# Optimization experiments

Measured on AMD Instinct MI355X. Metric: run time of the kernel, lower is better.

## Reference

```python
import jax, jax.numpy as jnp
import numpy as np

B, F, D, H, E, K = 4, 2048, 1024, 2048, 8, 2  # batch, frames, dim, expert hidden, n_experts, top_k


def setup_inputs() -> dict:
    key = jax.random.key(0)
    ks = jax.random.split(key, 9)
    sc = lambda k, shape, fan_in: (jax.random.normal(k, shape, jnp.float32) * (fan_in ** -0.5))
    return {
        "x": jax.random.normal(ks[0], (B, F, D), jnp.float32),
        # router: Linear(D,D) -> SiLU -> Linear(D,E)
        "rw1": sc(ks[1], (D, D), D),
        "rb1": jnp.zeros((D,), jnp.float32),
        "rw2": sc(ks[2], (D, E), D),
        "rb2": jnp.zeros((E,), jnp.float32),
        # experts: E x (Linear(D,H) -> SiLU -> Linear(H,D))
        "ew1": sc(ks[3], (E, D, H), D),
        "eb1": jnp.zeros((E, H), jnp.float32),
        "ew2": sc(ks[4], (E, H, D), H),
        "eb2": jnp.zeros((E, D), jnp.float32),
    }


def reference(x, rw1, rb1, rw2, rb2, ew1, eb1, ew2, eb2):
    b, f, d = x.shape
    t = x.reshape(b * f, d)                                   # [T, D]
    # router (eval mode: no topk noise)
    logits = jax.nn.silu(t @ rw1 + rb1) @ rw2 + rb2            # [T, E]
    vals, idx = jax.lax.top_k(logits, K)                       # [T, K]
    rows = jnp.arange(t.shape[0])[:, None]
    masked = jnp.full_like(logits, -jnp.inf).at[rows, idx].set(vals)
    w = jax.nn.softmax(masked, axis=1)                         # [T, E], nonzero only on top-k
    # dense per-expert FFN, then weighted combine (residual: y starts as x)
    eh = jax.nn.silu(jnp.einsum('td,edh->teh', t, ew1) + eb1[None])   # [T, E, H]
    eo = jnp.einsum('teh,ehd->ted', eh, ew2) + eb2[None]              # [T, E, D]
    y = t + jnp.einsum('te,ted->td', w, eo)
    return y.reshape(b, f, d)
```

## Files before the change

### kernel.cpp

```cpp
#include <hip/hip_runtime.h>
#include <hip/hip_bf16.h>
#include <cstdint>
#include <cstddef>

#define T_TOK 8192
#define DDIM  1024
#define HDIM  2048
#define NEXP  8
#define TOPK  2
#define KAUG  (3 * DDIM)

typedef short bf16x8 __attribute__((ext_vector_type(8)));
typedef float f32x4  __attribute__((ext_vector_type(4)));

__device__ __forceinline__ unsigned short f2bf(float f) {
  union { float f; unsigned u; } v; v.f = f;
  unsigned r = v.u + 0x7FFFu + ((v.u >> 16) & 1u);
  return (unsigned short)(r >> 16);
}
__device__ __forceinline__ float bf2f(unsigned short h) {
  union { unsigned u; float f; } v; v.u = ((unsigned)h) << 16;
  return v.f;
}
__device__ __forceinline__ float silu_fast(float v) {
  return v / (1.0f + __expf(-v));
}
__device__ __forceinline__ float silu_precise(float v) {
  return v / (1.0f + expf(-v));
}

__device__ __forceinline__ void gload16(const unsigned short* g, unsigned short* l) {
  __builtin_amdgcn_global_load_lds(
      (const __attribute__((address_space(1))) unsigned int*)g,
      (__attribute__((address_space(3))) unsigned int*)l,
      16, 0, 0);
}

__global__ void split_x_kernel(const float* __restrict__ in,
                               unsigned short* __restrict__ xaug, int n4) {
  int i = blockIdx.x * blockDim.x + threadIdx.x;
  if (i >= n4) return;
  float4 v = ((const float4*)in)[i];
  int t = i / (DDIM / 4);
  int kc = (i % (DDIM / 4)) * 4;
  float f[4] = {v.x, v.y, v.z, v.w};
  ushort4 hi, lo;
  unsigned short h[4], l[4];
#pragma unroll
  for (int j = 0; j < 4; j++) {
    h[j] = f2bf(f[j]);
    l[j] = f2bf(f[j] - bf2f(h[j]));
  }
  hi.x = h[0]; hi.y = h[1]; hi.z = h[2]; hi.w = h[3];
  lo.x = l[0]; lo.y = l[1]; lo.z = l[2]; lo.w = l[3];
  *(ushort4*)&xaug[(size_t)t * KAUG + kc] = hi;
  *(ushort4*)&xaug[(size_t)t * KAUG + DDIM + kc] = hi;
  *(ushort4*)&xaug[(size_t)t * KAUG + 2 * DDIM + kc] = lo;
}

__global__ __launch_bounds__(256) void split_w_kernel(
    const float* __restrict__ in, unsigned short* __restrict__ waug) {
  __shared__ float tile[32][33];
  int c0 = blockIdx.x * 32, r0 = blockIdx.y * 32;
  int tx = threadIdx.x & 31, ty = threadIdx.x >> 5;
#pragma unroll
  for (int i = 0; i < 32; i += 8)
    tile[ty + i][tx] = in[(size_t)(r0 + ty + i) * DDIM + (c0 + tx)];
  __syncthreads();
#pragma unroll
  for (int i = 0; i < 32; i += 8) {
    float v = tile[tx][ty + i];
    unsigned short h = f2bf(v);
    unsigned short l = f2bf(v - bf2f(h));
    int n = c0 + ty + i, k = r0 + tx;
    waug[(size_t)n * KAUG + k] = h;
    waug[(size_t)n * KAUG + DDIM + k] = l;
    waug[(size_t)n * KAUG + 2 * DDIM + k] = h;
  }
}

__global__ __launch_bounds__(256) void transpose_conv_kernel(
    const float* __restrict__ in, unsigned short* __restrict__ out, int R, int C) {
  __shared__ float tile[32][33];
  const int z = blockIdx.z;
  const float* src = in + (size_t)z * R * C;
  unsigned short* dst = out + (size_t)z * R * C;
  int c0 = blockIdx.x * 32, r0 = blockIdx.y * 32;
  int tx = threadIdx.x & 31, ty = threadIdx.x >> 5;
#pragma unroll
  for (int i = 0; i < 32; i += 8)
    tile[ty + i][tx] = src[(size_t)(r0 + ty + i) * C + (c0 + tx)];
  __syncthreads();
#pragma unroll
  for (int i = 0; i < 32; i += 8)
    dst[(size_t)(c0 + ty + i) * R + (r0 + tx)] = f2bf(tile[tx][ty + i]);
}

__global__ void zero_small_kernel(int* __restrict__ counts, int* __restrict__ cursors) {
  int i = threadIdx.x;
  if (i < NEXP) { counts[i] = 0; cursors[i] = 0; }
}

template <int EPI>
__global__ __launch_bounds__(256) void gemm_mfma(
    const unsigned short* __restrict__ Abase,
    const unsigned short* __restrict__ Btbase,
    const float* __restrict__ bias,
    float* __restrict__ outF,
    unsigned short* __restrict__ outBf,
    const int* __restrict__ toks,
    const int* __restrict__ offs, const int* __restrict__ cnts,
    int N, int KD, int Astride, int numE, int nTiles, int mCap) {
  const int id = blockIdx.x;
  const int e = id % numE;
  const int r = id / numE;
  const int n0 = (r % nTiles) * 128;
  const int mb = r / nTiles;

  int ne = T_TOK, off = 0;
  if (EPI != 0) { ne = cnts[e]; off = offs[e]; }

  const unsigned short* Bt = Btbase + (size_t)e * N * KD;
  const unsigned short* A = (EPI == 2) ? (Abase + (size_t)off * Astride) : Abase;

  __shared__ unsigned short As[2][128][32];
  __shared__ unsigned short Bs[2][128][32];

  const int tid  = threadIdx.x;
  const int lane = tid & 63, wid = tid >> 6;
  const int wm = wid >> 1, wn = wid & 1;
  const int quad = lane >> 4, l16 = lane & 15;

  const int rowS0 = tid >> 2;
  const int kc0 = (tid & 3) * 8;

  const size_t brow0 = (size_t)(n0 + rowS0) * KD;
  const size_t brow1 = brow0 + (size_t)64 * KD;
  const int nIter = KD / 32;
  const int mStride = mCap * 128;

  for (int m0 = mb * 128; m0 < ne; m0 += mStride) {
    size_t arow0, arow1;
    if (EPI == 1) {
      int p0 = m0 + rowS0, p1 = m0 + rowS0 + 64;
      int t0 = (p0 < ne) ? toks[off + p0] : 0;
      int t1 = (p1 < ne) ? toks[off + p1] : 0;
      arow0 = (size_t)t0 * Astride;
      arow1 = (size_t)t1 * Astride;
    } else if (EPI == 2) {
      arow0 = (size_t)min(m0 + rowS0, ne - 1) * Astride;
      arow1 = (size_t)min(m0 + rowS0 + 64, ne - 1) * Astride;
    } else {
      arow0 = (size_t)(m0 + rowS0) * Astride;
      arow1 = arow0 + (size_t)64 * Astride;
    }

    f32x4 zf = {0.f, 0.f, 0.f, 0.f};
    f32x4 acc[4][4];
#pragma unroll
    for (int mi = 0; mi < 4; mi++)
#pragma unroll
      for (int ni = 0; ni < 4; ni++) acc[mi][ni] = zf;

    {
      unsigned short* a0 = &As[0][0][0] + wid * 512;
      unsigned short* b0 = &Bs[0][0][0] + wid * 512;
      gload16(A + arow0 + kc0, a0);
      gload16(A + arow1 + kc0, a0 + 2048);
      gload16(Bt + brow0 + kc0, b0);
      gload16(Bt + brow1 + kc0, b0 + 2048);
    }

    for (int k = 0; k < nIter; k++) {
      const int cur = k & 1;
      if (k + 1 < nIter) {
        const int nk = (k + 1) * 32;
        unsigned short* a0 = &As[cur ^ 1][0][0] + wid * 512;
        unsigned short* b0 = &Bs[cur ^ 1][0][0] + wid * 512;
        gload16(A + arow0 + nk + kc0, a0);
        gload16(A + arow1 + nk + kc0, a0 + 2048);
        gload16(Bt + brow0 + nk + kc0, b0);
        gload16(Bt + brow1 + nk + kc0, b0 + 2048);
        __builtin_amdgcn_s_waitcnt(0x0F74);
      } else {
        __builtin_amdgcn_s_waitcnt(0x0F70);
      }
      __builtin_amdgcn_s_barrier();
      bf16x8 af[4], bfr[4];
#pragma unroll
      for (int mi = 0; mi < 4; mi++)
        af[mi] = *(const bf16x8*)&As[cur][wm * 64 + mi * 16 + l16][quad * 8];
#pragma unroll
      for (int ni = 0; ni < 4; ni++)
        bfr[ni] = *(const bf16x8*)&Bs[cur][wn * 64 + ni * 16 + l16][quad * 8];
#pragma unroll
      for (int mi = 0; mi < 4; mi++)
#pragma unroll
        for (int ni = 0; ni < 4; ni++)
          acc[mi][ni] = __builtin_amdgcn_mfma_f32_16x16x32_bf16(
              af[mi], bfr[ni], acc[mi][ni], 0, 0, 0);
      __builtin_amdgcn_s_barrier();
    }

#pragma unroll
    for (int mi = 0; mi < 4; mi++) {
      const int prow_base = wm * 64 + mi * 16 + quad * 4;
#pragma unroll
      for (int rr = 0; rr < 4; rr++) {
        const int p = m0 + prow_base + rr;
        if (EPI != 0 && p >= ne) continue;
#pragma unroll
        for (int ni = 0; ni < 4; ni++) {
          const int col = n0 + wn * 64 + ni * 16 + l16;
          float v = acc[mi][ni][rr] + bias[(size_t)e * N + col];
          if (EPI == 0) {
            outF[(size_t)p * N + col] = silu_precise(v);
          } else if (EPI == 1) {
            outBf[(size_t)(off + p) * N + col] = f2bf(silu_fast(v));
          } else {
            outBf[(size_t)(off + p) * N + col] = f2bf(v);
          }
        }
      }
    }
  }
}

__global__ __launch_bounds__(256) void router2_kernel(
    const float* __restrict__ rh, const float* __restrict__ rw2,
    const float* __restrict__ rb2, float* __restrict__ logits) {
  int t = blockIdx.x * 4 + (threadIdx.x >> 6);
  int lane = threadIdx.x & 63;
  const float* row = rh + (size_t)t * DDIM;
  float acc[NEXP];
#pragma unroll
  for (int e = 0; e < NEXP; e++) acc[e] = 0.f;
  for (int k = lane; k < DDIM; k += 64) {
    float v = row[k];
    const float* w = rw2 + (size_t)k * NEXP;
#pragma unroll
    for (int e = 0; e < NEXP; e++) acc[e] += v * w[e];
  }
#pragma unroll
  for (int e = 0; e < NEXP; e++) {
#pragma unroll
    for (int off = 32; off > 0; off >>= 1) acc[e] += __shfl_xor(acc[e], off, 64);
  }
#pragma unroll
  for (int e = 0; e < NEXP; e++)
    if (lane == e) logits[(size_t)t * NEXP + e] = acc[e] + rb2[e];
}

__global__ void topk_kernel(const float* __restrict__ logits,
                            int* __restrict__ idx2, float* __restrict__ w2arr,
                            int* __restrict__ counts) {
  int t = blockIdx.x * blockDim.x + threadIdx.x;
  if (t >= T_TOK) return;
  float l[NEXP];
#pragma unroll
  for (int e = 0; e < NEXP; e++) l[e] = logits[(size_t)t * NEXP + e];
  int i1 = 0; float v1 = l[0];
#pragma unroll
  for (int e = 1; e < NEXP; e++)
    if (l[e] > v1) { v1 = l[e]; i1 = e; }
  int i2 = -1; float v2 = -3.4e38f;
#pragma unroll
  for (int e = 0; e < NEXP; e++)
    if (e != i1 && l[e] > v2) { v2 = l[e]; i2 = e; }
  float ex = expf(v2 - v1);
  float wa = 1.f / (1.f + ex);
  float wb = ex / (1.f + ex);
  idx2[t * 2] = i1; idx2[t * 2 + 1] = i2;
  w2arr[t * 2] = wa; w2arr[t * 2 + 1] = wb;
  atomicAdd(&counts[i1], 1);
  atomicAdd(&counts[i2], 1);
}

__global__ void prefix_kernel(const int* __restrict__ counts, int* __restrict__ offs) {
  if (threadIdx.x == 0 && blockIdx.x == 0) {
    int s = 0;
    for (int e = 0; e < NEXP; e++) { offs[e] = s; s += counts[e]; }
  }
}

__global__ void scatter_kernel(const int* __restrict__ idx2,
                               const int* __restrict__ offs, int* __restrict__ cursors,
                               int* __restrict__ toks, int* __restrict__ posArr) {
  int t = blockIdx.x * blockDim.x + threadIdx.x;
  if (t >= T_TOK) return;
#pragma unroll
  for (int j = 0; j < TOPK; j++) {
    int e = idx2[t * 2 + j];
    int pos = atomicAdd(&cursors[e], 1);
    int s = offs[e] + pos;
    toks[s] = t;
    posArr[t * 2 + j] = s;
  }
}

__global__ __launch_bounds__(256) void combine_kernel(
    const float* __restrict__ x, const unsigned short* __restrict__ eo,
    const int* __restrict__ posArr, const float* __restrict__ w2arr,
    float* __restrict__ y) {
  const int t = blockIdx.x;
  const int d = threadIdx.x * 4;
  const int s0 = posArr[t * 2], s1 = posArr[t * 2 + 1];
  const float w0 = w2arr[t * 2], w1 = w2arr[t * 2 + 1];
  float4 xv = *(const float4*)&x[(size_t)t * DDIM + d];
  ushort4 a = *(const ushort4*)&eo[(size_t)s0 * DDIM + d];
  ushort4 b = *(const ushort4*)&eo[(size_t)s1 * DDIM + d];
  float4 o;
  o.x = xv.x + w0 * bf2f(a.x) + w1 * bf2f(b.x);
  o.y = xv.y + w0 * bf2f(a.y) + w1 * bf2f(b.y);
  o.z = xv.z + w0 * bf2f(a.z) + w1 * bf2f(b.z);
  o.w = xv.w + w0 * bf2f(a.w) + w1 * bf2f(b.w);
  *(float4*)&y[(size_t)t * DDIM + d] = o;
}

extern "C" void kernel_launch(void* const* d_in, const int* in_sizes, int n_in,
                              void* d_out, int out_size, void* d_ws, size_t ws_size,
                              hipStream_t stream) {
  (void)in_sizes; (void)n_in; (void)out_size; (void)ws_size;
  const float* x   = (const float*)d_in[0];
  const float* rw1 = (const float*)d_in[1];
  const float* rb1 = (const float*)d_in[2];
  const float* rw2 = (const float*)d_in[3];
  const float* rb2 = (const float*)d_in[4];
  const float* ew1 = (const float*)d_in[5];
  const float* eb1 = (const float*)d_in[6];
  const float* ew2 = (const float*)d_in[7];
  const float* eb2 = (const float*)d_in[8];
  float* y = (float*)d_out;

  char* ws = (char*)d_ws;
  size_t o = 0;
  auto alloc = [&](size_t bytes) {
    size_t r = o;
    o += (bytes + 255) & ~(size_t)255;
    return r;
  };
  unsigned short* xaug  = (unsigned short*)(ws + alloc((size_t)T_TOK * KAUG * 2));
  unsigned short* waug  = (unsigned short*)(ws + alloc((size_t)DDIM * KAUG * 2));
  unsigned short* ew1t  = (unsigned short*)(ws + alloc((size_t)NEXP * HDIM * DDIM * 2));
  unsigned short* ew2t  = (unsigned short*)(ws + alloc((size_t)NEXP * DDIM * HDIM * 2));
  float*          rh    = (float*)(ws + alloc((size_t)T_TOK * DDIM * 4));
  float*          logits= (float*)(ws + alloc((size_t)T_TOK * NEXP * 4));
  int*            idx2  = (int*)(ws + alloc((size_t)T_TOK * 2 * 4));
  float*          w2    = (float*)(ws + alloc((size_t)T_TOK * 2 * 4));
  int*            toks  = (int*)(ws + alloc((size_t)T_TOK * TOPK * 4));
  int*            posArr= (int*)(ws + alloc((size_t)T_TOK * TOPK * 4));
  int*            counts= (int*)(ws + alloc(256));
  int*            cursors=(int*)(ws + alloc(256));
  int*            offs  = (int*)(ws + alloc(256));
  unsigned short* ehb   = (unsigned short*)(ws + alloc((size_t)T_TOK * TOPK * HDIM * 2));
  unsigned short* eo    = (unsigned short*)(ws + alloc((size_t)T_TOK * TOPK * DDIM * 2));

  zero_small_kernel<<<1, 64, 0, stream>>>(counts, cursors);

  const int n4 = T_TOK * DDIM / 4;
  split_x_kernel<<<(n4 + 255) / 256, 256, 0, stream>>>(x, xaug, n4);
  split_w_kernel<<<dim3(DDIM / 32, DDIM / 32), 256, 0, stream>>>(rw1, waug);
  transpose_conv_kernel<<<dim3(HDIM / 32, DDIM / 32, NEXP), 256, 0, stream>>>(ew1, ew1t, DDIM, HDIM);
  transpose_conv_kernel<<<dim3(DDIM / 32, HDIM / 32, NEXP), 256, 0, stream>>>(ew2, ew2t, HDIM, DDIM);

  gemm_mfma<0><<<512, 256, 0, stream>>>(
      xaug, waug, rb1, rh, nullptr, nullptr, nullptr, nullptr,
      DDIM, KAUG, KAUG, 1, 8, 64);
  router2_kernel<<<T_TOK / 4, 256, 0, stream>>>(rh, rw2, rb2, logits);
  topk_kernel<<<T_TOK / 256, 256, 0, stream>>>(logits, idx2, w2, counts);
  prefix_kernel<<<1, 64, 0, stream>>>(counts, offs);
  scatter_kernel<<<T_TOK / 256, 256, 0, stream>>>(idx2, offs, cursors, toks, posArr);

  gemm_mfma<1><<<8 * 16 * 16, 256, 0, stream>>>(
      xaug, ew1t, eb1, nullptr, ehb, toks, offs, counts,
      HDIM, DDIM, KAUG, NEXP, 16, 16);
  gemm_mfma<2><<<8 * 8 * 32, 256, 0, stream>>>(
      ehb, ew2t, eb2, nullptr, eo, nullptr, offs, counts,
      DDIM, HDIM, HDIM, NEXP, 8, 32);
  combine_kernel<<<T_TOK, 256, 0, stream>>>(x, eo, posArr, w2, y);
}
```

Baseline: 804.9 us.

## Use plain bf16 router GEMM with fp32 fixup for near-tie tokens

Drops the three-term split-bf16 emulation of the fp32 router GEMM and runs it in plain bf16, which cuts the router GEMM K dimension by a factor of three and shrinks the x/weight staging buffers. To keep expert selection correct, tokens whose second and third logits fall within a small margin are flagged and recomputed in full fp32 by a new fixup kernel, which patches the indices, weights and counts. The prefix kernel is removed and offsets are recomputed inline from counts. This risks mis-routing tokens whose bf16 error exceeds the tie margin, and the fixup cost grows with the number of flagged tokens.

After: 1.078 ms. 1.34x slower.

```diff
diff --git a/kernel.cpp b/kernel.cpp
--- a/kernel.cpp
+++ b/kernel.cpp
@@ -8,7 +8,7 @@
 #define HDIM  2048
 #define NEXP  8
 #define TOPK  2
-#define KAUG  (3 * DDIM)
+#define TIE_DELTA 0.05f
 
 typedef short bf16x8 __attribute__((ext_vector_type(8)));
 typedef float f32x4  __attribute__((ext_vector_type(4)));
@@ -36,47 +36,14 @@
       16, 0, 0);
 }
 
-__global__ void split_x_kernel(const float* __restrict__ in,
-                               unsigned short* __restrict__ xaug, int n4) {
+__global__ void conv_x_kernel(const float* __restrict__ in,
+                              unsigned short* __restrict__ out, int n4) {
   int i = blockIdx.x * blockDim.x + threadIdx.x;
   if (i >= n4) return;
   float4 v = ((const float4*)in)[i];
-  int t = i / (DDIM / 4);
-  int kc = (i % (DDIM / 4)) * 4;
-  float f[4] = {v.x, v.y, v.z, v.w};
-  ushort4 hi, lo;
-  unsigned short h[4], l[4];
-#pragma unroll
-  for (int j = 0; j < 4; j++) {
-    h[j] = f2bf(f[j]);
-    l[j] = f2bf(f[j] - bf2f(h[j]));
-  }
-  hi.x = h[0]; hi.y = h[1]; hi.z = h[2]; hi.w = h[3];
-  lo.x = l[0]; lo.y = l[1]; lo.z = l[2]; lo.w = l[3];
-  *(ushort4*)&xaug[(size_t)t * KAUG + kc] = hi;
-  *(ushort4*)&xaug[(size_t)t * KAUG + DDIM + kc] = hi;
-  *(ushort4*)&xaug[(size_t)t * KAUG + 2 * DDIM + kc] = lo;
-}
-
-__global__ __launch_bounds__(256) void split_w_kernel(
-    const float* __restrict__ in, unsigned short* __restrict__ waug) {
-  __shared__ float tile[32][33];
-  int c0 = blockIdx.x * 32, r0 = blockIdx.y * 32;
-  int tx = threadIdx.x & 31, ty = threadIdx.x >> 5;
-#pragma unroll
-  for (int i = 0; i < 32; i += 8)
-    tile[ty + i][tx] = in[(size_t)(r0 + ty + i) * DDIM + (c0 + tx)];
-  __syncthreads();
-#pragma unroll
-  for (int i = 0; i < 32; i += 8) {
-    float v = tile[tx][ty + i];
-    unsigned short h = f2bf(v);
-    unsigned short l = f2bf(v - bf2f(h));
-    int n = c0 + ty + i, k = r0 + tx;
-    waug[(size_t)n * KAUG + k] = h;
-    waug[(size_t)n * KAUG + DDIM + k] = l;
-    waug[(size_t)n * KAUG + 2 * DDIM + k] = h;
-  }
+  ushort4 o;
+  o.x = f2bf(v.x); o.y = f2bf(v.y); o.z = f2bf(v.z); o.w = f2bf(v.w);
+  ((ushort4*)out)[i] = o;
 }
 
 __global__ __launch_bounds__(256) void transpose_conv_kernel(
@@ -96,9 +63,11 @@
     dst[(size_t)(c0 + ty + i) * R + (r0 + tx)] = f2bf(tile[tx][ty + i]);
 }
 
-__global__ void zero_small_kernel(int* __restrict__ counts, int* __restrict__ cursors) {
+__global__ void zero_small_kernel(int* __restrict__ counts, int* __restrict__ cursors,
+                                  int* __restrict__ flagCnt) {
   int i = threadIdx.x;
   if (i < NEXP) { counts[i] = 0; cursors[i] = 0; }
+  if (i == NEXP) *flagCnt = 0;
 }
 
 template <int EPI>
@@ -109,7 +78,7 @@
     float* __restrict__ outF,
     unsigned short* __restrict__ outBf,
     const int* __restrict__ toks,
-    const int* __restrict__ offs, const int* __restrict__ cnts,
+    const int* __restrict__ cnts,
     int N, int KD, int Astride, int numE, int nTiles, int mCap) {
   const int id = blockIdx.x;
   const int e = id % numE;
@@ -118,7 +87,13 @@
   const int mb = r / nTiles;
 
   int ne = T_TOK, off = 0;
-  if (EPI != 0) { ne = cnts[e]; off = offs[e]; }
+  if (EPI != 0) {
+    for (int q = 0; q < NEXP; q++) {
+      int c = cnts[q];
+      if (q < e) off += c;
+      if (q == e) ne = c;
+    }
+  }
 
   const unsigned short* Bt = Btbase + (size_t)e * N * KD;
   const unsigned short* A = (EPI == 2) ? (Abase + (size_t)off * Astride) : Abase;
@@ -253,7 +228,8 @@
 
 __global__ void topk_kernel(const float* __restrict__ logits,
                             int* __restrict__ idx2, float* __restrict__ w2arr,
-                            int* __restrict__ counts) {
+                            int* __restrict__ counts,
+                            int* __restrict__ flagList, int* __restrict__ flagCnt) {
   int t = blockIdx.x * blockDim.x + threadIdx.x;
   if (t >= T_TOK) return;
   float l[NEXP];
@@ -267,6 +243,10 @@
 #pragma unroll
   for (int e = 0; e < NEXP; e++)
     if (e != i1 && l[e] > v2) { v2 = l[e]; i2 = e; }
+  float v3 = -3.4e38f;
+#pragma unroll
+  for (int e = 0; e < NEXP; e++)
+    if (e != i1 && e != i2 && l[e] > v3) v3 = l[e];
   float ex = expf(v2 - v1);
   float wa = 1.f / (1.f + ex);
   float wb = ex / (1.f + ex);
@@ -274,27 +254,95 @@
   w2arr[t * 2] = wa; w2arr[t * 2 + 1] = wb;
   atomicAdd(&counts[i1], 1);
   atomicAdd(&counts[i2], 1);
-}
-
-__global__ void prefix_kernel(const int* __restrict__ counts, int* __restrict__ offs) {
-  if (threadIdx.x == 0 && blockIdx.x == 0) {
-    int s = 0;
-    for (int e = 0; e < NEXP; e++) { offs[e] = s; s += counts[e]; }
+  if (v2 - v3 < TIE_DELTA) {
+    int pos = atomicAdd(flagCnt, 1);
+    flagList[pos] = t;
+  }
+}
+
+__global__ __launch_bounds__(256) void fixup_kernel(
+    const float* __restrict__ x, const float* __restrict__ rw1,
+    const float* __restrict__ rb1, const float* __restrict__ rw2,
+    const float* __restrict__ rb2,
+    const int* __restrict__ flagList, const int* __restrict__ flagCnt,
+    int* __restrict__ idx2, float* __restrict__ w2arr, int* __restrict__ counts) {
+  __shared__ float xs[DDIM];
+  __shared__ float part[4][NEXP];
+  const int n = *flagCnt;
+  const int tid = threadIdx.x;
+  const int lane = tid & 63, wid = tid >> 6;
+  for (int i = blockIdx.x; i < n; i += gridDim.x) {
+    const int t = flagList[i];
+    for (int k = tid; k < DDIM; k += 256) xs[k] = x[(size_t)t * DDIM + k];
+    __syncthreads();
+    const int j0 = tid * 4;
+    float h0 = rb1[j0], h1 = rb1[j0 + 1], h2 = rb1[j0 + 2], h3 = rb1[j0 + 3];
+    for (int k = 0; k < DDIM; k++) {
+      float xv = xs[k];
+      float4 wv = *(const float4*)(rw1 + (size_t)k * DDIM + j0);
+      h0 += xv * wv.x; h1 += xv * wv.y; h2 += xv * wv.z; h3 += xv * wv.w;
+    }
+    h0 = silu_precise(h0); h1 = silu_precise(h1);
+    h2 = silu_precise(h2); h3 = silu_precise(h3);
+    float acc[NEXP];
+#pragma unroll
+    for (int e = 0; e < NEXP; e++) {
+      acc[e] = h0 * rw2[(size_t)j0 * NEXP + e] + h1 * rw2[(size_t)(j0 + 1) * NEXP + e]
+             + h2 * rw2[(size_t)(j0 + 2) * NEXP + e] + h3 * rw2[(size_t)(j0 + 3) * NEXP + e];
+    }
+#pragma unroll
+    for (int e = 0; e < NEXP; e++)
+#pragma unroll
+      for (int off = 32; off > 0; off >>= 1) acc[e] += __shfl_xor(acc[e], off, 64);
+    if (lane == 0)
+#pragma unroll
+      for (int e = 0; e < NEXP; e++) part[wid][e] = acc[e];
+    __syncthreads();
+    if (tid == 0) {
+      float l[NEXP];
+#pragma unroll
+      for (int e = 0; e < NEXP; e++)
+        l[e] = rb2[e] + part[0][e] + part[1][e] + part[2][e] + part[3][e];
+      int i1 = 0; float v1 = l[0];
+#pragma unroll
+      for (int e = 1; e < NEXP; e++)
+        if (l[e] > v1) { v1 = l[e]; i1 = e; }
+      int i2 = -1; float v2 = -3.4e38f;
+#pragma unroll
+      for (int e = 0; e < NEXP; e++)
+        if (e != i1 && l[e] > v2) { v2 = l[e]; i2 = e; }
+      float ex = expf(v2 - v1);
+      float wa = 1.f / (1.f + ex);
+      float wb = ex / (1.f + ex);
+      int o0 = idx2[t * 2], o1 = idx2[t * 2 + 1];
+      bool same = ((o0 == i1 && o1 == i2) || (o0 == i2 && o1 == i1));
+      if (!same) {
+        atomicSub(&counts[o0], 1); atomicSub(&counts[o1], 1);
+        atomicAdd(&counts[i1], 1); atomicAdd(&counts[i2], 1);
+      }
+      idx2[t * 2] = i1; idx2[t * 2 + 1] = i2;
+      w2arr[t * 2] = wa; w2arr[t * 2 + 1] = wb;
+    }
+    __syncthreads();
   }
 }
 
 __global__ void scatter_kernel(const int* __restrict__ idx2,
-                               const int* __restrict__ offs, int* __restrict__ cursors,
+                               const int* __restrict__ counts, int* __restrict__ cursors,
                                int* __restrict__ toks, int* __restrict__ posArr) {
   int t = blockIdx.x * blockDim.x + threadIdx.x;
   if (t >= T_TOK) return;
+  int offs[NEXP];
+  int s = 0;
+#pragma unroll
+  for (int e = 0; e < NEXP; e++) { offs[e] = s; s += counts[e]; }
 #pragma unroll
   for (int j = 0; j < TOPK; j++) {
     int e = idx2[t * 2 + j];
     int pos = atomicAdd(&cursors[e], 1);
-    int s = offs[e] + pos;
-    toks[s] = t;
-    posArr[t * 2 + j] = s;
+    int sl = offs[e] + pos;
+    toks[sl] = t;
+    posArr[t * 2 + j] = sl;
   }
 }
 
@@ -339,8 +387,8 @@
     o += (bytes + 255) & ~(size_t)255;
     return r;
   };
-  unsigned short* xaug  = (unsigned short*)(ws + alloc((size_t)T_TOK * KAUG * 2));
-  unsigned short* waug  = (unsigned short*)(ws + alloc((size_t)DDIM * KAUG * 2));
+  unsigned short* xb    = (unsigned short*)(ws + alloc((size_t)T_TOK * DDIM * 2));
+  unsigned short* w1t   = (unsigned short*)(ws + alloc((size_t)DDIM * DDIM * 2));
   unsigned short* ew1t  = (unsigned short*)(ws + alloc((size_t)NEXP * HDIM * DDIM * 2));
   unsigned short* ew2t  = (unsigned short*)(ws + alloc((size_t)NEXP * DDIM * HDIM * 2));
   float*          rh    = (float*)(ws + alloc((size_t)T_TOK * DDIM * 4));
@@ -349,33 +397,35 @@
   float*          w2    = (float*)(ws + alloc((size_t)T_TOK * 2 * 4));
   int*            toks  = (int*)(ws + alloc((size_t)T_TOK * TOPK * 4));
   int*            posArr= (int*)(ws + alloc((size_t)T_TOK * TOPK * 4));
+  int*            flagL = (int*)(ws + alloc((size_t)T_TOK * 4));
   int*            counts= (int*)(ws + alloc(256));
   int*            cursors=(int*)(ws + alloc(256));
-  int*            offs  = (int*)(ws + alloc(256));
+  int*            flagC = (int*)(ws + alloc(256));
   unsigned short* ehb   = (unsigned short*)(ws + alloc((size_t)T_TOK * TOPK * HDIM * 2));
   unsigned short* eo    = (unsigned short*)(ws + alloc((size_t)T_TOK * TOPK * DDIM * 2));
 
-  zero_small_kernel<<<1, 64, 0, stream>>>(counts, cursors);
+  zero_small_kernel<<<1, 64, 0, stream>>>(counts, cursors, flagC);
 
   const int n4 = T_TOK * DDIM / 4;
-  split_x_kernel<<<(n4 + 255) / 256, 256, 0, stream>>>(x, xaug, n4);
-  split_w_kernel<<<dim3(DDIM / 32, DDIM / 32), 256, 0, stream>>>(rw1, waug);
+  conv_x_kernel<<<(n4 + 255) / 256, 256, 0, stream>>>(x, xb, n4);
+  transpose_conv_kernel<<<dim3(DDIM / 32, DDIM / 32, 1), 256, 0, stream>>>(rw1, w1t, DDIM, DDIM);
   transpose_conv_kernel<<<dim3(HDIM / 32, DDIM / 32, NEXP), 256, 0, stream>>>(ew1, ew1t, DDIM, HDIM);
   transpose_conv_kernel<<<dim3(DDIM / 32, HDIM / 32, NEXP), 256, 0, stream>>>(ew2, ew2t, HDIM, DDIM);
 
   gemm_mfma<0><<<512, 256, 0, stream>>>(
-      xaug, waug, rb1, rh, nullptr, nullptr, nullptr, nullptr,
-      DDIM, KAUG, KAUG, 1, 8, 64);
+      xb, w1t, rb1, rh, nullptr, nullptr, nullptr,
+      DDIM, DDIM, DDIM, 1, 8, 64);
   router2_kernel<<<T_TOK / 4, 256, 0, stream>>>(rh, rw2, rb2, logits);
-  topk_kernel<<<T_TOK / 256, 256, 0, stream>>>(logits, idx2, w2, counts);
-  prefix_kernel<<<1, 64, 0, stream>>>(counts, offs);
-  scatter_kernel<<<T_TOK / 256, 256, 0, stream>>>(idx2, offs, cursors, toks, posArr);
+  topk_kernel<<<T_TOK / 256, 256, 0, stream>>>(logits, idx2, w2, counts, flagL, flagC);
+  fixup_kernel<<<256, 256, 0, stream>>>(x, rw1, rb1, rw2, rb2, flagL, flagC,
+                                        idx2, w2, counts);
+  scatter_kernel<<<T_TOK / 256, 256, 0, stream>>>(idx2, counts, cursors, toks, posArr);
 
   gemm_mfma<1><<<8 * 16 * 16, 256, 0, stream>>>(
-      xaug, ew1t, eb1, nullptr, ehb, toks, offs, counts,
-      HDIM, DDIM, KAUG, NEXP, 16, 16);
+      xb, ew1t, eb1, nullptr, ehb, toks, counts,
+      HDIM, DDIM, DDIM, NEXP, 16, 16);
   gemm_mfma<2><<<8 * 8 * 32, 256, 0, stream>>>(
-      ehb, ew2t, eb2, nullptr, eo, nullptr, offs, counts,
+      ehb, ew2t, eb2, nullptr, eo, nullptr, counts,
       DDIM, HDIM, HDIM, NEXP, 8, 32);
   combine_kernel<<<T_TOK, 256, 0, stream>>>(x, eo, posArr, w2, y);
 }
```
